# Kernel optimization log

Hardware: AMD Instinct MI355X
Metric: run time of the kernel (lower is better)

Reference implementation:

```python
import jax, jax.numpy as jnp
import numpy as np

D_IN = 256
D_OUT = 256

def setup_inputs() -> dict:
    key = jax.random.key(0)
    kx, kq, kk, kv = jax.random.split(key, 4)
    x = jax.random.normal(kx, (8, D_IN, 64, 64), dtype=jnp.float32)
    s = 1.0 / np.sqrt(D_IN)
    Wq = jax.random.normal(kq, (D_OUT, D_IN), dtype=jnp.float32) * s
    Wk = jax.random.normal(kk, (D_OUT, D_IN), dtype=jnp.float32) * s
    Wv = jax.random.normal(kv, (D_OUT, D_IN), dtype=jnp.float32) * s
    return {"x": x, "Wq": Wq, "Wk": Wk, "Wv": Wv}

def reference(x, Wq, Wk, Wv):
    b, c_in, h, w = x.shape
    c = Wq.shape[0]
    # 1x1 conv == channel linear; tokens along N = h*w
    xt = x.reshape(b, c_in, h * w).transpose(0, 2, 1)      # (b, N, c_in)
    q = jnp.einsum('bnc,dc->bnd', xt, Wq)                  # (b, N, c)
    k = jnp.einsum('bnc,dc->bnd', xt, Wk)
    v = jnp.einsum('bnc,dc->bnd', xt, Wv)
    wei = jnp.einsum('bnd,bmd->bnm', q, k) / jnp.sqrt(jnp.asarray(c, x.dtype))
    wei = jax.nn.softmax(wei, axis=-1)
    out = jnp.einsum('bnm,bmd->bnd', wei, v)               # (b, N, c)
    return out.transpose(0, 2, 1).reshape(b, c, h, w)
```

## Files before the change

kernel.cpp:

```cpp
#include <hip/hip_runtime.h>

#define DIN 256
#define NTOK 4096

typedef __bf16 bf16;
typedef __bf16 bf16x4 __attribute__((ext_vector_type(4)));
typedef __bf16 bf16x8 __attribute__((ext_vector_type(8)));
typedef float floatx16 __attribute__((ext_vector_type(16)));

__device__ inline floatx16 mfma32(bf16x8 a, bf16x8 b, floatx16 c) {
    return __builtin_amdgcn_mfma_f32_32x32x16_bf16(a, b, c, 0, 0, 0);
}

__device__ inline void async16(const void* g, void* l) {
    __builtin_amdgcn_global_load_lds(
        (const __attribute__((address_space(1))) unsigned int*)g,
        (__attribute__((address_space(3))) unsigned int*)l, 16, 0, 0);
}

__global__ void convert_w(const float* __restrict__ wq, const float* __restrict__ wk,
                          const float* __restrict__ wv, bf16* __restrict__ Wb) {
    int i = blockIdx.x * 256 + threadIdx.x;
    const float* src = (i < 65536) ? wq : (i < 131072 ? wk : wv);
    Wb[i] = (bf16)src[i & 65535];
}

__global__ __launch_bounds__(256, 2) void proj_kernel(
    const float* __restrict__ x, const bf16* __restrict__ Wb,
    bf16* __restrict__ Qo, bf16* __restrict__ Ko, bf16* __restrict__ Vo)
{
    __shared__ bf16 xs[64][264];
    __shared__ bf16 wsm[64][264];

    int bid = blockIdx.x;
    int b = bid & 7, nt = bid >> 3;
    int n0 = nt * 64;
    int t = threadIdx.x;
    int lane = t & 63, w = t >> 6;
    int l32 = lane & 31, h = lane >> 5;
    int tokg = w >> 1;
    int og   = w & 1;

    {
        const float* xb = x + (size_t)b * DIN * NTOK;
#pragma unroll
        for (int it = 0; it < 16; ++it) {
            int flat = it * 256 + t;
            int c = flat >> 4;
            int nf = flat & 15;
            float4 v = *(const float4*)(xb + (size_t)c * NTOK + n0 + nf * 4);
            int nn = nf * 4;
            xs[nn + 0][c] = (bf16)v.x;
            xs[nn + 1][c] = (bf16)v.y;
            xs[nn + 2][c] = (bf16)v.z;
            xs[nn + 3][c] = (bf16)v.w;
        }
    }
    __syncthreads();

    bf16x8 xf[16];
#pragma unroll
    for (int ks = 0; ks < 16; ++ks)
        xf[ks] = *(const bf16x8*)&xs[tokg * 32 + l32][ks * 16 + h * 8];

    for (int mat = 0; mat < 3; ++mat) {
        const bf16* Wm = Wb + mat * 65536;
        for (int dg = 0; dg < 4; ++dg) {
            __syncthreads();
#pragma unroll
            for (int it = 0; it < 8; ++it) {
                int flat = it * 256 + t;
                int r = flat >> 5;
                int cs = (flat & 31) * 8;
                *(bf16x8*)&wsm[r][cs] =
                    *(const bf16x8*)(Wm + (size_t)(dg * 64 + r) * 256 + cs);
            }
            __syncthreads();

            floatx16 acc;
#pragma unroll
            for (int i = 0; i < 16; ++i) acc[i] = 0.0f;

            if (mat < 2) {
#pragma unroll
                for (int ks = 0; ks < 16; ++ks) {
                    bf16x8 wf = *(const bf16x8*)&wsm[og * 32 + l32][ks * 16 + h * 8];
                    acc = mfma32(xf[ks], wf, acc);
                }
                bf16* Out = (mat == 0 ? Qo : Ko) + (size_t)b * NTOK * DIN;
                int d = dg * 64 + og * 32 + l32;
#pragma unroll
                for (int r = 0; r < 16; ++r) {
                    int tok = n0 + tokg * 32 + (r & 3) + 8 * (r >> 2) + 4 * h;
                    Out[(size_t)tok * DIN + d] = (bf16)acc[r];
                }
            } else {
#pragma unroll
                for (int ks = 0; ks < 16; ++ks) {
                    bf16x8 wf = *(const bf16x8*)&wsm[og * 32 + l32][ks * 16 + h * 8];
                    acc = mfma32(wf, xf[ks], acc);
                }
                bf16* Out = Vo + (size_t)b * DIN * NTOK;
                int tok = n0 + tokg * 32 + l32;
#pragma unroll
                for (int r = 0; r < 16; ++r) {
                    int d = dg * 64 + og * 32 + (r & 3) + 8 * (r >> 2) + 4 * h;
                    Out[(size_t)d * NTOK + tok] = (bf16)acc[r];
                }
            }
        }
    }
}

__global__ __launch_bounds__(512, 2) void attn_kernel(
    const bf16* __restrict__ Q, const bf16* __restrict__ K,
    const bf16* __restrict__ V, float* __restrict__ out)
{
    __shared__ bf16 Ks[2][64][256];
    __shared__ bf16 Vs[2][256][64];
    __shared__ bf16 Ps[2][128][64];

    int bid = blockIdx.x;
    int b = bid & 7, qt = bid >> 3;
    int n0 = qt * 128;
    int t = threadIdx.x, lane = t & 63, w = t >> 6;
    int l32 = lane & 31, h = lane >> 5;
    int lkey = (l32 & 7) ^ ((l32 >> 3) & 3);

    const bf16* Qb = Q + (size_t)b * NTOK * DIN;
    const bf16* Kb = K + (size_t)b * NTOK * DIN;
    const bf16* Vb = V + (size_t)b * DIN * NTOK;
    float* Lp = (float*)&Ps[0][0][0];

    if (w < 4) {
        int tokg = w >> 1, mg = w & 1;
        int krow = mg * 32 + l32;

        int koff[8];
#pragma unroll
        for (int jj = 0; jj < 8; ++jj) {
            int q = w * 8 + jj;
            int r = q * 2 + (lane >> 5);
            int ck = (lane & 31) ^ ((r & 7) ^ ((r >> 3) & 3));
            koff[jj] = (r * 256 + ck * 8) * 2;
        }

        bf16x8 qf[2][16];
#pragma unroll
        for (int ca = 0; ca < 2; ++ca) {
            const bf16* qrow = Qb + (size_t)(n0 + tokg * 64 + ca * 32 + l32) * DIN + h * 8;
#pragma unroll
            for (int ks = 0; ks < 16; ++ks) qf[ca][ks] = *(const bf16x8*)(qrow + ks * 16);
        }

        float lsum[2] = {0.0f, 0.0f};

#pragma unroll
        for (int jj = 0; jj < 8; ++jj) {
            async16((const char*)Kb + koff[jj], (bf16*)Ks[0] + (w * 8 + jj) * 512);
            async16((const char*)Kb + 32768 + koff[jj], (bf16*)Ks[1] + (w * 8 + jj) * 512);
        }
        __syncthreads();

        {
            const bf16* Krd = (const bf16*)Ks[0] + krow * 256;
            floatx16 st[2];
#pragma unroll
            for (int i = 0; i < 16; ++i) { st[0][i] = 0.0f; st[1][i] = 0.0f; }
#pragma unroll
            for (int ks = 0; ks < 16; ++ks) {
                bf16x8 kf = *(const bf16x8*)(Krd + (((2 * ks + h) ^ lkey) * 8));
                st[0] = mfma32(kf, qf[0][ks], st[0]);
                st[1] = mfma32(kf, qf[1][ks], st[1]);
            }
#pragma unroll
            for (int ca = 0; ca < 2; ++ca) {
                bf16* Prow = (bf16*)Ps[0] + (tokg * 64 + ca * 32 + l32) * 64;
                float tsum = 0.0f;
#pragma unroll
                for (int g = 0; g < 4; ++g) {
                    bf16x4 pk;
#pragma unroll
                    for (int i = 0; i < 4; ++i) {
                        float e = __expf(st[ca][g * 4 + i] * 0.0625f);
                        tsum += e;
                        pk[i] = (bf16)e;
                    }
                    *(bf16x4*)((char*)Prow + (((mg * 4 + g) ^ lkey) * 16) + h * 8) = pk;
                }
                lsum[ca] += tsum;
            }
        }
        __syncthreads();

        for (int mt = 0; mt < 64; ++mt) {
            if (mt < 62) {
                int kadd = (mt + 2) * 32768;
#pragma unroll
                for (int jj = 0; jj < 8; ++jj)
                    async16((const char*)Kb + kadd + koff[jj],
                            (bf16*)Ks[mt & 1] + (w * 8 + jj) * 512);
            }
            if (mt < 63) {
                const bf16* Krd = (const bf16*)Ks[(mt + 1) & 1] + krow * 256;
                floatx16 st[2];
#pragma unroll
                for (int i = 0; i < 16; ++i) { st[0][i] = 0.0f; st[1][i] = 0.0f; }
#pragma unroll
                for (int ks = 0; ks < 16; ++ks) {
                    bf16x8 kf = *(const bf16x8*)(Krd + (((2 * ks + h) ^ lkey) * 8));
                    st[0] = mfma32(kf, qf[0][ks], st[0]);
                    st[1] = mfma32(kf, qf[1][ks], st[1]);
                }
                bf16* Pw = (bf16*)Ps[(mt + 1) & 1];
#pragma unroll
                for (int ca = 0; ca < 2; ++ca) {
                    bf16* Prow = Pw + (tokg * 64 + ca * 32 + l32) * 64;
                    float tsum = 0.0f;
#pragma unroll
                    for (int g = 0; g < 4; ++g) {
                        bf16x4 pk;
#pragma unroll
                        for (int i = 0; i < 4; ++i) {
                            float e = __expf(st[ca][g * 4 + i] * 0.0625f);
                            tsum += e;
                            pk[i] = (bf16)e;
                        }
                        *(bf16x4*)((char*)Prow + (((mg * 4 + g) ^ lkey) * 16) + h * 8) = pk;
                    }
                    lsum[ca] += tsum;
                }
            }
            __syncthreads();
        }

#pragma unroll
        for (int ca = 0; ca < 2; ++ca) {
            float sv = lsum[ca];
            sv += __shfl_xor(sv, 32);
            if (h == 0) Lp[mg * 128 + tokg * 64 + ca * 32 + l32] = sv;
        }
        __syncthreads();
    } else {
        int slab = w - 4;

        int vofs[8];
#pragma unroll
        for (int jj = 0; jj < 8; ++jj) {
            int q = slab * 8 + jj;
            int d = q * 8 + (lane >> 3);
            int cv = (lane & 7) ^ ((d & 7) ^ ((d >> 3) & 3));
            vofs[jj] = (d * 4096 + cv * 8) * 2;
        }

        floatx16 oacc[8];
#pragma unroll
        for (int i = 0; i < 8; ++i)
            for (int j = 0; j < 16; ++j) oacc[i][j] = 0.0f;

#pragma unroll
        for (int jj = 0; jj < 8; ++jj)
            async16((const char*)Vb + vofs[jj], (bf16*)Vs[0] + (slab * 8 + jj) * 512);
        __syncthreads();
        __syncthreads();

        for (int mt = 0; mt < 64; ++mt) {
            if (mt < 63) {
                int vadd = (mt + 1) * 128;
#pragma unroll
                for (int jj = 0; jj < 8; ++jj)
                    async16((const char*)Vb + vadd + vofs[jj],
                            (bf16*)Vs[(mt + 1) & 1] + (slab * 8 + jj) * 512);
            }
            const bf16* Vrd = (const bf16*)Vs[mt & 1];
            const char* Prd = (const char*)Ps[mt & 1];
#pragma unroll
            for (int kst = 0; kst < 4; ++kst) {
                bf16x8 va[2], pb[4];
#pragma unroll
                for (int dc = 0; dc < 2; ++dc) {
                    int d = slab * 64 + dc * 32 + l32;
                    va[dc] = *(const bf16x8*)(Vrd + d * 64 + (((kst * 2 + h) ^ lkey) * 8));
                }
#pragma unroll
                for (int tc = 0; tc < 4; ++tc)
                    pb[tc] = *(const bf16x8*)(Prd + (tc * 32 + l32) * 128 +
                                              (((kst * 2 + h) ^ lkey) * 16));
#pragma unroll
                for (int dc = 0; dc < 2; ++dc)
#pragma unroll
                    for (int tc = 0; tc < 4; ++tc)
                        oacc[dc * 4 + tc] = mfma32(va[dc], pb[tc], oacc[dc * 4 + tc]);
            }
            __syncthreads();
        }

        __syncthreads();
        float* ob = out + (size_t)b * DIN * NTOK;
#pragma unroll
        for (int tc = 0; tc < 4; ++tc) {
            int tok = tc * 32 + l32;
            float rinv = 1.0f / (Lp[tok] + Lp[128 + tok]);
#pragma unroll
            for (int dc = 0; dc < 2; ++dc)
#pragma unroll
                for (int r = 0; r < 16; ++r) {
                    int d = slab * 64 + dc * 32 + (r & 3) + 8 * (r >> 2) + 4 * h;
                    ob[(size_t)d * NTOK + n0 + tok] = oacc[dc * 4 + tc][r] * rinv;
                }
        }
    }
}

extern "C" void kernel_launch(void* const* d_in, const int* in_sizes, int n_in,
                              void* d_out, int out_size, void* d_ws, size_t ws_size,
                              hipStream_t stream) {
    const float* x  = (const float*)d_in[0];
    const float* wq = (const float*)d_in[1];
    const float* wk = (const float*)d_in[2];
    const float* wv = (const float*)d_in[3];
    float* outf = (float*)d_out;

    char* ws = (char*)d_ws;
    bf16* Wb = (bf16*)(ws);
    bf16* Qp = (bf16*)(ws + (1u << 20));
    bf16* Kp = (bf16*)(ws + (1u << 20) + (16u << 20));
    bf16* Vp = (bf16*)(ws + (1u << 20) + (32u << 20));

    convert_w<<<768, 256, 0, stream>>>(wq, wk, wv, Wb);
    proj_kernel<<<512, 256, 0, stream>>>(x, Wb, Qp, Kp, Vp);
    attn_kernel<<<256, 512, 0, stream>>>(Qp, Kp, Vp, outf);
}
```

Measured before the change: 240.4 us.

## Double-buffer weight tiles in projection kernel with async global-to-LDS loads

Replaces the synchronous weight tile staging in the QKV projection kernel with double-buffered global_load_lds async copies, prefetching the next 64-row weight tile while computing the current one. The LDS layout is XOR-swizzled to avoid bank conflicts on the MFMA fragment reads, and one buffer aliases the x staging area to keep the LDS footprint the same. This hides weight-load latency behind compute and removes one barrier per tile. The risks are that no explicit wait on the async loads (vmcnt) may be present before the barrier, and that the projection kernel is likely only a small part of total time compared with attention.

```diff
diff --git a/kernel.cpp b/kernel.cpp
--- a/kernel.cpp
+++ b/kernel.cpp
@@ -29,8 +29,10 @@
     const float* __restrict__ x, const bf16* __restrict__ Wb,
     bf16* __restrict__ Qo, bf16* __restrict__ Ko, bf16* __restrict__ Vo)
 {
-    __shared__ bf16 xs[64][264];
-    __shared__ bf16 wsm[64][264];
+    __shared__ __attribute__((aligned(16))) char smem[33792 + 32768];
+    bf16 (*xs)[264] = (bf16(*)[264])smem;
+    bf16* bufB = (bf16*)smem;
+    bf16* bufA = (bf16*)(smem + 33792);
 
     int bid = blockIdx.x;
     int b = bid & 7, nt = bid >> 3;
@@ -38,8 +40,18 @@
     int t = threadIdx.x;
     int lane = t & 63, w = t >> 6;
     int l32 = lane & 31, h = lane >> 5;
+    int hl = lane >> 5;
     int tokg = w >> 1;
     int og   = w & 1;
+
+    int wofs[8];
+#pragma unroll
+    for (int jj = 0; jj < 8; ++jj) {
+        int q = w * 8 + jj;
+        int r2 = 2 * q + hl;
+        int cs = (l32) ^ (r2 & 31);
+        wofs[jj] = r2 * 512 + cs * 16;
+    }
 
     {
         const float* xb = x + (size_t)b * DIN * NTOK;
@@ -58,57 +70,65 @@
     }
     __syncthreads();
 
+    {
+        const char* src = (const char*)Wb;
+#pragma unroll
+        for (int jj = 0; jj < 8; ++jj)
+            async16(src + wofs[jj], (char*)bufA + (w * 8 + jj) * 1024);
+    }
+
     bf16x8 xf[16];
 #pragma unroll
     for (int ks = 0; ks < 16; ++ks)
         xf[ks] = *(const bf16x8*)&xs[tokg * 32 + l32][ks * 16 + h * 8];
 
-    for (int mat = 0; mat < 3; ++mat) {
-        const bf16* Wm = Wb + mat * 65536;
-        for (int dg = 0; dg < 4; ++dg) {
-            __syncthreads();
-#pragma unroll
-            for (int it = 0; it < 8; ++it) {
-                int flat = it * 256 + t;
-                int r = flat >> 5;
-                int cs = (flat & 31) * 8;
-                *(bf16x8*)&wsm[r][cs] =
-                    *(const bf16x8*)(Wm + (size_t)(dg * 64 + r) * 256 + cs);
-            }
-            __syncthreads();
-
-            floatx16 acc;
-#pragma unroll
-            for (int i = 0; i < 16; ++i) acc[i] = 0.0f;
-
-            if (mat < 2) {
-#pragma unroll
-                for (int ks = 0; ks < 16; ++ks) {
-                    bf16x8 wf = *(const bf16x8*)&wsm[og * 32 + l32][ks * 16 + h * 8];
-                    acc = mfma32(xf[ks], wf, acc);
-                }
-                bf16* Out = (mat == 0 ? Qo : Ko) + (size_t)b * NTOK * DIN;
-                int d = dg * 64 + og * 32 + l32;
-#pragma unroll
-                for (int r = 0; r < 16; ++r) {
-                    int tok = n0 + tokg * 32 + (r & 3) + 8 * (r >> 2) + 4 * h;
-                    Out[(size_t)tok * DIN + d] = (bf16)acc[r];
-                }
-            } else {
-#pragma unroll
-                for (int ks = 0; ks < 16; ++ks) {
-                    bf16x8 wf = *(const bf16x8*)&wsm[og * 32 + l32][ks * 16 + h * 8];
-                    acc = mfma32(wf, xf[ks], acc);
-                }
-                bf16* Out = Vo + (size_t)b * DIN * NTOK;
-                int tok = n0 + tokg * 32 + l32;
-#pragma unroll
-                for (int r = 0; r < 16; ++r) {
-                    int d = dg * 64 + og * 32 + (r & 3) + 8 * (r >> 2) + 4 * h;
-                    Out[(size_t)d * NTOK + tok] = (bf16)acc[r];
-                }
-            }
-        }
+    __syncthreads();
+
+    for (int p = 0; p < 12; ++p) {
+        if (p < 11) {
+            bf16* nb = ((p + 1) & 1) ? bufB : bufA;
+            const char* src = (const char*)Wb + (size_t)(p + 1) * 32768;
+#pragma unroll
+            for (int jj = 0; jj < 8; ++jj)
+                async16(src + wofs[jj], (char*)nb + (w * 8 + jj) * 1024);
+        }
+
+        const bf16* wb = (p & 1) ? bufB : bufA;
+        const bf16* Wrd = wb + (og * 32 + l32) * 256;
+        int mat = p >> 2, dg = p & 3;
+
+        floatx16 acc;
+#pragma unroll
+        for (int i = 0; i < 16; ++i) acc[i] = 0.0f;
+
+        if (mat < 2) {
+#pragma unroll
+            for (int ks = 0; ks < 16; ++ks) {
+                bf16x8 wf = *(const bf16x8*)(Wrd + (((2 * ks + h) ^ l32) * 8));
+                acc = mfma32(xf[ks], wf, acc);
+            }
+            bf16* Out = (mat == 0 ? Qo : Ko) + (size_t)b * NTOK * DIN;
+            int d = dg * 64 + og * 32 + l32;
+#pragma unroll
+            for (int r = 0; r < 16; ++r) {
+                int tok = n0 + tokg * 32 + (r & 3) + 8 * (r >> 2) + 4 * h;
+                Out[(size_t)tok * DIN + d] = (bf16)acc[r];
+            }
+        } else {
+#pragma unroll
+            for (int ks = 0; ks < 16; ++ks) {
+                bf16x8 wf = *(const bf16x8*)(Wrd + (((2 * ks + h) ^ l32) * 8));
+                acc = mfma32(wf, xf[ks], acc);
+            }
+            bf16* Out = Vo + (size_t)b * DIN * NTOK;
+            int tok = n0 + tokg * 32 + l32;
+#pragma unroll
+            for (int r = 0; r < 16; ++r) {
+                int d = dg * 64 + og * 32 + (r & 3) + 8 * (r >> 2) + 4 * h;
+                Out[(size_t)d * NTOK + tok] = (bf16)acc[r];
+            }
+        }
+        __syncthreads();
     }
 }
 
```

Result: no change. 238.5 us (-0.8%).
